# Kernel optimization log

Hardware: AMD Instinct MI355X
Metric: run time of the kernel (lower is better)

## Reference

```python
import jax, jax.numpy as jnp
import numpy as np

L = 880      # flattened RootMLP param count: (1*8+8) + (8*96+96)
HID = 8      # MLP hidden width
OUT = 96     # 2*data_size
DS = 48      # data_size
T = 64       # sequence length
BATCH = 4


def setup_inputs() -> dict:
    key = jax.random.key(0)
    k1, k2, k3, k4, k5 = jax.random.split(key, 5)
    xs = jax.random.normal(k1, (BATCH, T, DS), jnp.float32)
    ts = jax.random.uniform(k2, (BATCH, T), dtype=jnp.float32)
    theta0 = 0.1 * jax.random.normal(k3, (L,), jnp.float32)
    # near-identity A so matrix powers up to A^(T-1) stay bounded
    A = 0.99 * jnp.eye(L, dtype=jnp.float32) + (0.01 / np.sqrt(L)) * jax.random.normal(k4, (L, L), jnp.float32)
    B = 0.01 * jax.random.normal(k5, (L, DS), jnp.float32)
    return {"xs": xs, "ts": ts, "theta0": theta0, "A": A, "B": B, "aux": 0}


def _forward(xs, ts, theta0, A, B):
    Bt, T_, _ = xs.shape
    I = jnp.eye(L, dtype=A.dtype)

    # A_pows[t] = A^t for t = 0..T-1, via a cumulative matmul scan
    def step(P, _):
        return P @ A, P
    _, pows = jax.lax.scan(step, I, None, length=T_)  # (T, L, L)

    # K_conv = [B, A^0(A-I)B, ..., A^(T-3)(A-I)B]  -> (T-1, L, DS)
    M = (A - I) @ B
    K_tail = jnp.einsum('tij,jd->tid', pows[:T_ - 2], M)
    K_conv = jnp.concatenate([B[None], K_tail], axis=0)

    # FFT circular convolution of input signal with K_conv over time
    u = xs[:, 1:, :]                      # (B, T-1, DS)
    u_f = jnp.fft.fft(u, axis=1)
    K_f = jnp.fft.fft(K_conv, axis=0)     # (T-1, L, DS)
    thetas = jnp.fft.ifft(jnp.einsum('tld,btd->btl', K_f, u_f), axis=1).real

    # initial-condition convolution with K_conv0 = A^tau, tau = 0..T-2
    K0 = pows[:T_ - 1]                    # (T-1, L, L)
    sig = jnp.zeros((Bt, T_ - 1, L), xs.dtype)
    sig = sig.at[:, 0, :].set(theta0)
    sig = sig.at[:, 1, :].set(-(xs[:, 0, :] @ B.T))
    sig_f = jnp.fft.fft(sig, axis=1)
    K0_f = jnp.fft.fft(K0, axis=0)
    phi0 = jnp.fft.ifft(jnp.einsum('tlm,btm->btl', K0_f, sig_f), axis=1).real

    thetas = thetas + phi0
    thetas = jnp.concatenate([jnp.broadcast_to(theta0, (Bt, 1, L)), thetas], axis=1)  # (B, T, L)

    # apply RootMLP (1 -> HID -> OUT) with params unflattened from thetas
    W0 = thetas[..., :HID]                                    # (B,T,HID): W0 is (HID,1)
    b0 = thetas[..., HID:2 * HID]
    W1 = thetas[..., 2 * HID:2 * HID + OUT * HID].reshape(Bt, T_, OUT, HID)
    b1 = thetas[..., 2 * HID + OUT * HID:]
    h = jax.nn.relu(W0 * ts[..., None] + b0)                  # (B,T,HID)
    out = jnp.einsum('btoh,bth->bto', W1, h) + b1             # (B,T,OUT)
    # reconstruction head: tanh means, softplus stds
    return jnp.concatenate([jnp.tanh(out[..., :DS]), jax.nn.softplus(out[..., DS:])], axis=-1)


def reference(xs, ts, theta0, A, B, aux):
    return _forward(xs, ts, theta0, A, B)
```

## Files before the change

### kernel.cpp

```cpp
#include <hip/hip_runtime.h>
#include <math.h>

typedef unsigned int uint;
typedef unsigned short ushort;
typedef short s16x8 __attribute__((ext_vector_type(8)));
typedef float f32x4 __attribute__((ext_vector_type(4)));
typedef uint u32x4 __attribute__((ext_vector_type(4)));

#define L     880
#define LP    896
#define NC    64
#define WSZ   (NC * LP)
#define DS    48
#define OUTD  96
#define KCV   3072
#define NZ    6

#define OFF_E    0
#define OFF_KDT  0
#define OFF_WF   4415488
#define OFF_WB   (OFF_WF + 32 * WSZ)
#define OFF_U    (OFF_WB + 32 * WSZ / 2)
#define OFF_PART (OFF_U + 256 * KCV / 2)
#define OFF_PHI  (OFF_PART + NZ * 256 * LP)

#define LROW 72
#define LBUF (64 * LROW)
#define LGRP (2 * LBUF)

__device__ inline ushort f2b(float f) {
  uint u = __builtin_bit_cast(uint, f);
  u += 0x7fffu + ((u >> 16) & 1u);
  return (ushort)(u >> 16);
}
__device__ inline float b2f(ushort b) {
  uint u = ((uint)b) << 16;
  return __builtin_bit_cast(float, u);
}

__device__ __forceinline__ void mma_core(const ushort* __restrict__ aptr,
                                         const ushort* __restrict__ bptr,
                                         int KH, int tid, ushort* ldsA, ushort* ldsB,
                                         f32x4 acc[2][2]) {
  const int grp = tid >> 8;
  const int t2  = tid & 255;
  const int gL  = grp * LGRP;
  const int r = t2 >> 2, kq = (t2 & 3) * 16;
  const int wv = t2 >> 6, lane = tid & 63;
  const int wm = (wv >> 1) * 32, wn = (wv & 1) * 32;
  const int lr = lane & 15, lg = lane >> 4;
  acc[0][0] = f32x4{0.f, 0.f, 0.f, 0.f};
  acc[0][1] = f32x4{0.f, 0.f, 0.f, 0.f};
  acc[1][0] = f32x4{0.f, 0.f, 0.f, 0.f};
  acc[1][1] = f32x4{0.f, 0.f, 0.f, 0.f};
  u32x4 ra0 = *(const u32x4*)aptr;
  u32x4 ra1 = *(const u32x4*)(aptr + 8);
  u32x4 rb0 = *(const u32x4*)bptr;
  u32x4 rb1 = *(const u32x4*)(bptr + 8);
  __syncthreads();
  *(u32x4*)&ldsA[gL + r * LROW + kq]     = ra0;
  *(u32x4*)&ldsA[gL + r * LROW + kq + 8] = ra1;
  *(u32x4*)&ldsB[gL + r * LROW + kq]     = rb0;
  *(u32x4*)&ldsB[gL + r * LROW + kq + 8] = rb1;
  if (KH > 1) {
    ra0 = *(const u32x4*)(aptr + 64);  ra1 = *(const u32x4*)(aptr + 72);
    rb0 = *(const u32x4*)(bptr + 64);  rb1 = *(const u32x4*)(bptr + 72);
  }
  __syncthreads();
  for (int it = 0; it < KH; ++it) {
    const int cur = gL + (it & 1) * LBUF;
    const int nxt = gL + ((it & 1) ^ 1) * LBUF;
    s16x8 fa0[2], fa1[2], fb0[2], fb1[2];
#pragma unroll
    for (int k2 = 0; k2 < 2; ++k2) {
      fa0[k2] = *(const s16x8*)&ldsA[cur + (wm + lr) * LROW + k2 * 32 + lg * 8];
      fa1[k2] = *(const s16x8*)&ldsA[cur + (wm + 16 + lr) * LROW + k2 * 32 + lg * 8];
      fb0[k2] = *(const s16x8*)&ldsB[cur + (wn + lr) * LROW + k2 * 32 + lg * 8];
      fb1[k2] = *(const s16x8*)&ldsB[cur + (wn + 16 + lr) * LROW + k2 * 32 + lg * 8];
    }
    if (it + 1 < KH) {
      *(u32x4*)&ldsA[nxt + r * LROW + kq]     = ra0;
      *(u32x4*)&ldsA[nxt + r * LROW + kq + 8] = ra1;
      *(u32x4*)&ldsB[nxt + r * LROW + kq]     = rb0;
      *(u32x4*)&ldsB[nxt + r * LROW + kq + 8] = rb1;
      if (it + 2 < KH) {
        ra0 = *(const u32x4*)(aptr + (it + 2) * 64);
        ra1 = *(const u32x4*)(aptr + (it + 2) * 64 + 8);
        rb0 = *(const u32x4*)(bptr + (it + 2) * 64);
        rb1 = *(const u32x4*)(bptr + (it + 2) * 64 + 8);
      }
    }
#pragma unroll
    for (int k2 = 0; k2 < 2; ++k2) {
      acc[0][0] = __builtin_amdgcn_mfma_f32_16x16x32_bf16(fa0[k2], fb0[k2], acc[0][0], 0, 0, 0);
      acc[0][1] = __builtin_amdgcn_mfma_f32_16x16x32_bf16(fa0[k2], fb1[k2], acc[0][1], 0, 0, 0);
      acc[1][0] = __builtin_amdgcn_mfma_f32_16x16x32_bf16(fa1[k2], fb0[k2], acc[1][0], 0, 0, 0);
      acc[1][1] = __builtin_amdgcn_mfma_f32_16x16x32_bf16(fa1[k2], fb1[k2], acc[1][1], 0, 0, 0);
    }
    __syncthreads();
  }
  float* red = (float*)ldsA;
  if (grp == 1) {
#pragma unroll
    for (int m = 0; m < 2; ++m)
#pragma unroll
      for (int n = 0; n < 2; ++n)
#pragma unroll
        for (int rr = 0; rr < 4; ++rr)
          red[((m * 2 + n) * 4 + rr) * 256 + t2] = acc[m][n][rr];
  }
  __syncthreads();
  if (grp == 0) {
#pragma unroll
    for (int m = 0; m < 2; ++m)
#pragma unroll
      for (int n = 0; n < 2; ++n)
#pragma unroll
        for (int rr = 0; rr < 4; ++rr)
          acc[m][n][rr] += red[((m * 2 + n) * 4 + rr) * 256 + t2];
  }
}

__device__ __forceinline__ void mma_core_f32A(const float* __restrict__ ap1,
                                              const float* __restrict__ ap0,
                                              const ushort* __restrict__ bptr,
                                              int KH, int tid, ushort* ldsA, ushort* ldsB,
                                              f32x4 acc[2][2]) {
  const int grp = tid >> 8;
  const int t2  = tid & 255;
  const int gL  = grp * LGRP;
  const int r = t2 >> 2, kq = (t2 & 3) * 16;
  const int wv = t2 >> 6, lane = tid & 63;
  const int wm = (wv >> 1) * 32, wn = (wv & 1) * 32;
  const int lr = lane & 15, lg = lane >> 4;
  acc[0][0] = f32x4{0.f, 0.f, 0.f, 0.f};
  acc[0][1] = f32x4{0.f, 0.f, 0.f, 0.f};
  acc[1][0] = f32x4{0.f, 0.f, 0.f, 0.f};
  acc[1][1] = f32x4{0.f, 0.f, 0.f, 0.f};
  float4 ca[4], pa[4];
  auto issueA = [&](int it) {
#pragma unroll
    for (int i = 0; i < 4; ++i) {
      ca[i] = *(const float4*)(ap1 + it * 64 + i * 4);
      pa[i] = *(const float4*)(ap0 + it * 64 + i * 4);
    }
  };
  auto packA = [&](int buf) {
    union { ushort s[16]; u32x4 v[2]; } pk;
#pragma unroll
    for (int i = 0; i < 4; ++i) {
      pk.s[i * 4 + 0] = f2b(ca[i].x - pa[i].x);
      pk.s[i * 4 + 1] = f2b(ca[i].y - pa[i].y);
      pk.s[i * 4 + 2] = f2b(ca[i].z - pa[i].z);
      pk.s[i * 4 + 3] = f2b(ca[i].w - pa[i].w);
    }
    *(u32x4*)&ldsA[buf + r * LROW + kq]     = pk.v[0];
    *(u32x4*)&ldsA[buf + r * LROW + kq + 8] = pk.v[1];
  };
  u32x4 rb0 = *(const u32x4*)bptr;
  u32x4 rb1 = *(const u32x4*)(bptr + 8);
  issueA(0);
  __syncthreads();
  packA(gL);
  *(u32x4*)&ldsB[gL + r * LROW + kq]     = rb0;
  *(u32x4*)&ldsB[gL + r * LROW + kq + 8] = rb1;
  if (KH > 1) {
    rb0 = *(const u32x4*)(bptr + 64);
    rb1 = *(const u32x4*)(bptr + 72);
    issueA(1);
  }
  __syncthreads();
  for (int it = 0; it < KH; ++it) {
    const int cur = gL + (it & 1) * LBUF;
    const int nxt = gL + ((it & 1) ^ 1) * LBUF;
    s16x8 fa0[2], fa1[2], fb0[2], fb1[2];
#pragma unroll
    for (int k2 = 0; k2 < 2; ++k2) {
      fa0[k2] = *(const s16x8*)&ldsA[cur + (wm + lr) * LROW + k2 * 32 + lg * 8];
      fa1[k2] = *(const s16x8*)&ldsA[cur + (wm + 16 + lr) * LROW + k2 * 32 + lg * 8];
      fb0[k2] = *(const s16x8*)&ldsB[cur + (wn + lr) * LROW + k2 * 32 + lg * 8];
      fb1[k2] = *(const s16x8*)&ldsB[cur + (wn + 16 + lr) * LROW + k2 * 32 + lg * 8];
    }
    if (it + 1 < KH) {
      packA(nxt);
      *(u32x4*)&ldsB[nxt + r * LROW + kq]     = rb0;
      *(u32x4*)&ldsB[nxt + r * LROW + kq + 8] = rb1;
      if (it + 2 < KH) {
        rb0 = *(const u32x4*)(bptr + (it + 2) * 64);
        rb1 = *(const u32x4*)(bptr + (it + 2) * 64 + 8);
        issueA(it + 2);
      }
    }
#pragma unroll
    for (int k2 = 0; k2 < 2; ++k2) {
      acc[0][0] = __builtin_amdgcn_mfma_f32_16x16x32_bf16(fa0[k2], fb0[k2], acc[0][0], 0, 0, 0);
      acc[0][1] = __builtin_amdgcn_mfma_f32_16x16x32_bf16(fa0[k2], fb1[k2], acc[0][1], 0, 0, 0);
      acc[1][0] = __builtin_amdgcn_mfma_f32_16x16x32_bf16(fa1[k2], fb0[k2], acc[1][0], 0, 0, 0);
      acc[1][1] = __builtin_amdgcn_mfma_f32_16x16x32_bf16(fa1[k2], fb1[k2], acc[1][1], 0, 0, 0);
    }
    __syncthreads();
  }
  float* red = (float*)ldsA;
  if (grp == 1) {
#pragma unroll
    for (int m = 0; m < 2; ++m)
#pragma unroll
      for (int n = 0; n < 2; ++n)
#pragma unroll
        for (int rr = 0; rr < 4; ++rr)
          red[((m * 2 + n) * 4 + rr) * 256 + t2] = acc[m][n][rr];
  }
  __syncthreads();
  if (grp == 0) {
#pragma unroll
    for (int m = 0; m < 2; ++m)
#pragma unroll
      for (int n = 0; n < 2; ++n)
#pragma unroll
        for (int rr = 0; rr < 4; ++rr)
          acc[m][n][rr] += red[((m * 2 + n) * 4 + rr) * 256 + t2];
  }
}

__device__ __forceinline__ void kd_body(const float* __restrict__ WF, ushort* __restrict__ KDT,
                                        int j, int l0, int tid, float (*D)[65]) {
  __syncthreads();
  if (j < 63) {
    const float* Wj = WF + (size_t)j * WSZ;
    for (int e = tid; e < 48 * 64; e += 512) {
      int d = e >> 6, ll = e & 63;
      float v = Wj[d * LP + l0 + ll];
      if (j > 0) v -= Wj[-(int)WSZ + d * LP + l0 + ll];
      D[d][ll] = v;
    }
  } else {
    for (int e = tid; e < 48 * 64; e += 512) { int d = e >> 6, ll = e & 63; D[d][ll] = 0.f; }
  }
  __syncthreads();
  for (int e = tid; e < 48 * 64; e += 512) {
    int ll = e / 48, d = e - ll * 48;
    KDT[(size_t)(l0 + ll) * KCV + j * 48 + d] = f2b(D[d][ll]);
  }
}

__global__ __launch_bounds__(256) void k_prep(const float* __restrict__ A,
                                              const float* __restrict__ B,
                                              const float* __restrict__ th0,
                                              const float* __restrict__ xs,
                                              ushort* __restrict__ EN,
                                              ushort* __restrict__ ET,
                                              float* __restrict__ WF,
                                              ushort* __restrict__ WB,
                                              ushort* __restrict__ U) {
  const int blk = blockIdx.x;
  const int tid = threadIdx.x;
  if (blk < 196) {
    __shared__ float T[64][65];
    const int bi = (blk / 14) * 64, bj = (blk % 14) * 64;
    const int r = tid >> 2, c0 = (tid & 3) * 16;
    const int gi = bi + r;
#pragma unroll
    for (int q = 0; q < 4; ++q) {
      int c = c0 + q * 4, gj = bj + c;
      float4 v = {0.f, 0.f, 0.f, 0.f};
      if (gi < L && gj + 3 < L) {
        v = *(const float4*)(A + (size_t)gi * L + gj);
      } else if (gi < L) {
        if (gj + 0 < L) v.x = A[(size_t)gi * L + gj];
        if (gj + 1 < L) v.y = A[(size_t)gi * L + gj + 1];
        if (gj + 2 < L) v.z = A[(size_t)gi * L + gj + 2];
        if (gj + 3 < L) v.w = A[(size_t)gi * L + gj + 3];
      }
      if (gi == gj)     v.x -= 0.99f;
      if (gi == gj + 1) v.y -= 0.99f;
      if (gi == gj + 2) v.z -= 0.99f;
      if (gi == gj + 3) v.w -= 0.99f;
      T[r][c] = v.x; T[r][c + 1] = v.y; T[r][c + 2] = v.z; T[r][c + 3] = v.w;
    }
    __syncthreads();
    {
      union { ushort s[16]; u32x4 v[2]; } pk;
#pragma unroll
      for (int i = 0; i < 16; ++i) pk.s[i] = f2b(T[r][c0 + i]);
      *(u32x4*)(EN + (size_t)(bi + r) * LP + bj + c0)     = pk.v[0];
      *(u32x4*)(EN + (size_t)(bi + r) * LP + bj + c0 + 8) = pk.v[1];
    }
    {
      union { ushort s[16]; u32x4 v[2]; } pk;
#pragma unroll
      for (int i = 0; i < 16; ++i) pk.s[i] = f2b(T[c0 + i][r]);
      *(u32x4*)(ET + (size_t)(bj + r) * LP + bi + c0)     = pk.v[0];
      *(u32x4*)(ET + (size_t)(bj + r) * LP + bi + c0 + 8) = pk.v[1];
    }
  } else if (blk < 210) {
    int base = (blk - 196) * 4096;
    for (int e = tid; e < 4096; e += 256) {
      int idx = base + e;
      int c = idx / LP, l = idx % LP;
      float v = 0.f;
      if (l < L) {
        if (c < DS) v = B[l * DS + c];
        else if (c == DS) v = th0[l];
        else if (c < 53) {
          int b = c - 49;
          float s = 0.f;
          for (int d = 0; d < DS; ++d) s += B[l * DS + d] * xs[(b * 64) * DS + d];
          v = -s;
        }
      }
      WF[idx] = v;
      WB[idx] = f2b(v);
    }
  } else {
    int idx = ((blk - 210) * 256 + tid) * 4;
    int rr = idx / KCV, k = idx - rr * KCV;
    ushort4 v = {0, 0, 0, 0};
    if (rr < 252 && k < 3024) {
      int b = rr / 63, tau = rr - b * 63;
      int j = k / DS, d = k - j * DS;
      int s = tau - j; if (s < 0) s += 63;
      float4 x4 = *(const float4*)(xs + (size_t)(b * 64 + s + 1) * DS + d);
      v.x = f2b(x4.x); v.y = f2b(x4.y); v.z = f2b(x4.z); v.w = f2b(x4.w);
    }
    *(ushort4*)(U + idx) = v;
  }
}

__global__ __launch_bounds__(512, 4) void k_ladder(
    const ushort* __restrict__ sqA, const ushort* __restrict__ sqBT, float cs2,
    ushort* __restrict__ sqOutN, ushort* __restrict__ sqOutT, int ySq,
    int nCh, const ushort* __restrict__ chWB, const ushort* __restrict__ chE, float csc,
    const float* __restrict__ chWFsrc, float* __restrict__ chWFdst,
    ushort* __restrict__ chWBdst,
    int kdJ0, const float* __restrict__ kdWF, ushort* __restrict__ kdKDT) {
  __shared__ __align__(16) ushort ldsA[2 * LGRP];
  __shared__ __align__(16) ushort ldsB[2 * LGRP];
  const int tid = threadIdx.x;
  const int y = blockIdx.y;
  const int n0 = blockIdx.x * 64;
  const int t2 = tid & 255, grp = tid >> 8;
  const int r = t2 >> 2, kq = (t2 & 3) * 16;
  const int kg = grp * 448 + kq;
  const int wv = t2 >> 6, lane = tid & 63;
  const int wm = (wv >> 1) * 32, wn = (wv & 1) * 32;
  const int lr = lane & 15, lg = lane >> 4;

  if (y < ySq) {
    const int m0 = y * 64;
    f32x4 acc[2][2];
    mma_core(sqA + (size_t)(m0 + r) * LP + kg, sqBT + (size_t)(n0 + r) * LP + kg,
             7, tid, ldsA, ldsB, acc);
    ushort* T = ldsB;
    if (tid < 256) {
#pragma unroll
      for (int fm = 0; fm < 2; ++fm)
#pragma unroll
        for (int fn = 0; fn < 2; ++fn)
#pragma unroll
          for (int rr = 0; rr < 4; ++rr) {
            int mi = wm + fm * 16 + lg * 4 + rr;
            int ni = wn + fn * 16 + lr;
            float v = acc[fm][fn][rr] + cs2 * b2f(sqA[(size_t)(m0 + mi) * LP + n0 + ni]);
            ushort bv = f2b(v);
            sqOutN[(size_t)(m0 + mi) * LP + n0 + ni] = bv;
            T[ni * LROW + mi] = bv;
          }
    }
    __syncthreads();
    if (sqOutT && tid < 256) {
      const int nr = tid >> 2, ct0 = (tid & 3) * 16;
      u32x4 o0 = *(const u32x4*)&T[nr * LROW + ct0];
      u32x4 o1 = *(const u32x4*)&T[nr * LROW + ct0 + 8];
      *(u32x4*)(sqOutT + (size_t)(n0 + nr) * LP + m0 + ct0)     = o0;
      *(u32x4*)(sqOutT + (size_t)(n0 + nr) * LP + m0 + ct0 + 8) = o1;
    }
  } else if (y < ySq + nCh) {
    const int t = y - ySq;
    f32x4 acc[2][2];
    mma_core(chWB + (size_t)t * WSZ + (size_t)r * LP + kg,
             chE + (size_t)(n0 + r) * LP + kg, 7, tid, ldsA, ldsB, acc);
    if (tid < 256) {
      const float*  srcF = chWFsrc + (size_t)t * WSZ;
      float*        dstF = chWFdst + (size_t)t * WSZ;
      ushort*       dstB = chWBdst + (size_t)t * WSZ;
#pragma unroll
      for (int fm = 0; fm < 2; ++fm)
#pragma unroll
        for (int fn = 0; fn < 2; ++fn)
#pragma unroll
          for (int rr = 0; rr < 4; ++rr) {
            int mi = wm + fm * 16 + lg * 4 + rr;
            int ni = n0 + wn + fn * 16 + lr;
            float v = acc[fm][fn][rr] + csc * srcF[(size_t)mi * LP + ni];
            dstF[(size_t)mi * LP + ni] = v;
            dstB[(size_t)mi * LP + ni] = f2b(v);
          }
    }
  } else {
    int j = kdJ0 + (y - ySq - nCh);
    kd_body(kdWF, kdKDT, j, n0, tid, (float(*)[65])ldsA);
  }
}

__global__ __launch_bounds__(512, 4) void k_tail(
    const ushort* __restrict__ WB, const float* __restrict__ WF,
    const ushort* __restrict__ EN16, const ushort* __restrict__ EN32,
    float c16v, float c32v, float* __restrict__ PHI, ushort* __restrict__ KDT) {
  __shared__ __align__(16) ushort ldsA[2 * LGRP];
  __shared__ __align__(16) ushort ldsB[2 * LGRP];
  const int tid = threadIdx.x;
  const int y = blockIdx.y;
  const int n0 = blockIdx.x * 64;
  const int t2 = tid & 255, grp = tid >> 8;
  const int r = t2 >> 2, kq = (t2 & 3) * 16;
  const int kg = grp * 448 + kq;
  const int wv = t2 >> 6, lane = tid & 63;
  const int wm = (wv >> 1) * 32, wn = (wv & 1) * 32;
  const int lr = lane & 15, lg = lane >> 4;

  if (y < 3) {
    const int m0 = y * 64;
    int i = m0 + r; if (i > 154) i = 154;
    int t = i / 5, q = i - t * 5;
    f32x4 acc[2][2];
    mma_core(WB + (size_t)t * WSZ + (size_t)(48 + q) * LP + kg,
             EN32 + (size_t)(n0 + r) * LP + kg, 7, tid, ldsA, ldsB, acc);
    if (tid < 256) {
#pragma unroll
      for (int fm = 0; fm < 2; ++fm)
#pragma unroll
        for (int fn = 0; fn < 2; ++fn)
#pragma unroll
          for (int rr = 0; rr < 4; ++rr) {
            int mi = wm + fm * 16 + lg * 4 + rr;
            int ni = n0 + wn + fn * 16 + lr;
            int io = m0 + mi;
            int ic = io > 154 ? 154 : io;
            int tt = ic / 5, qq = ic - tt * 5;
            float v = acc[fm][fn][rr] + c32v * WF[(size_t)tt * WSZ + (size_t)(48 + qq) * LP + ni];
            PHI[(size_t)io * LP + ni] = v;
          }
    }
  } else if (y < 34) {
    const int kt = y - 3;
    const int s = (kt == 0) ? 16 : kt;
    const ushort* E = (kt == 0) ? EN16 : EN32;
    const float coef = (kt == 0) ? c16v : c32v;
    const int j = (kt == 0) ? 32 : kt + 32;
    const float* ap1 = WF + (size_t)s * WSZ + (size_t)r * LP + kg;
    f32x4 acc[2][2];
    mma_core_f32A(ap1, ap1 - WSZ, E + (size_t)(n0 + r) * LP + kg, 7, tid, ldsA, ldsB, acc);
    ushort* T = ldsB;
    if (tid < 256) {
#pragma unroll
      for (int fm = 0; fm < 2; ++fm)
#pragma unroll
        for (int fn = 0; fn < 2; ++fn)
#pragma unroll
          for (int rr = 0; rr < 4; ++rr) {
            int mi = wm + fm * 16 + lg * 4 + rr;
            if (mi < 48) {
              int ni = n0 + wn + fn * 16 + lr;
              float kds = WF[(size_t)s * WSZ + (size_t)mi * LP + ni]
                        - WF[(size_t)(s - 1) * WSZ + (size_t)mi * LP + ni];
              float v = acc[fm][fn][rr] + coef * kds;
              T[(wn + fn * 16 + lr) * LROW + mi] = f2b(v);
            }
          }
    }
    __syncthreads();
    if (tid < 384) {
      int row = tid / 6, seg = tid - row * 6;
      *(u32x4*)(KDT + (size_t)(n0 + row) * KCV + j * 48 + seg * 8)
          = *(const u32x4*)&T[row * LROW + seg * 8];
    }
  } else {
    int idx = y - 34;
    int j = (idx < 16) ? 16 + idx : 63;
    kd_body(WF, KDT, j, n0, tid, (float(*)[65])ldsA);
  }
}

__global__ __launch_bounds__(512, 4) void k_conv(const ushort* __restrict__ U,
                                                 const ushort* __restrict__ KDT,
                                                 float* __restrict__ part) {
  __shared__ __align__(16) ushort ldsA[2 * LGRP];
  __shared__ __align__(16) ushort ldsB[2 * LGRP];
  const int tid = threadIdx.x;
  const int n0 = blockIdx.x * 64, m0 = blockIdx.y * 64;
  const int t2 = tid & 255, grp = tid >> 8;
  const int r = t2 >> 2, kq = (t2 & 3) * 16;
  const int kgc = blockIdx.z * 512 + grp * 256 + kq;
  const int wv = t2 >> 6, lane = tid & 63;
  const int wm = (wv >> 1) * 32, wn = (wv & 1) * 32;
  const int lr = lane & 15, lg = lane >> 4;
  f32x4 acc[2][2];
  mma_core(U + (size_t)(m0 + r) * KCV + kgc, KDT + (size_t)(n0 + r) * KCV + kgc,
           4, tid, ldsA, ldsB, acc);
  if (tid < 256) {
    float* pp = part + (size_t)blockIdx.z * (256 * LP);
#pragma unroll
    for (int fm = 0; fm < 2; ++fm)
#pragma unroll
      for (int fn = 0; fn < 2; ++fn)
#pragma unroll
        for (int rr = 0; rr < 4; ++rr) {
          int m = m0 + wm + fm * 16 + lg * 4 + rr;
          int n = n0 + wn + fn * 16 + lr;
          pp[(size_t)m * LP + n] = acc[fm][fn][rr];
        }
  }
}

__global__ __launch_bounds__(256) void k_final(const float* __restrict__ part,
                                               const float* __restrict__ PHI,
                                               const float* __restrict__ WF,
                                               const float* __restrict__ th0,
                                               const float* __restrict__ ts,
                                               float* __restrict__ out) {
  __shared__ float th[LP];
  const int bt = blockIdx.x, b = bt >> 6, t = bt & 63;
  for (int l = threadIdx.x; l < LP; l += 256) {
    float v = 0.f;
    if (l < L) {
      if (t == 0) v = th0[l];
      else {
        int rr = b * 63 + (t - 1);
#pragma unroll
        for (int z = 0; z < NZ; ++z) v += part[(size_t)z * (256 * LP) + rr * LP + l];
        int tau = t - 1;
        v += (tau < 32) ? WF[(size_t)tau * WSZ + DS * LP + l]
                        : PHI[(size_t)((tau - 32) * 5) * LP + l];
        int tw = (tau + 62) % 63;
        v += (tw < 32) ? WF[(size_t)tw * WSZ + (49 + b) * LP + l]
                       : PHI[(size_t)((tw - 32) * 5 + 1 + b) * LP + l];
      }
    }
    th[l] = v;
  }
  __syncthreads();
  int o = threadIdx.x;
  if (o < OUTD) {
    float tv = ts[bt];
    float acc = th[784 + o];
#pragma unroll
    for (int i = 0; i < 8; ++i) {
      float h = fmaxf(th[i] * tv + th[8 + i], 0.f);
      acc += th[16 + o * 8 + i] * h;
    }
    float rs;
    if (o < DS) rs = tanhf(acc);
    else        rs = fmaxf(acc, 0.f) + log1pf(expf(-fabsf(acc)));
    out[bt * OUTD + o] = rs;
  }
}

extern "C" void kernel_launch(void* const* d_in, const int* in_sizes, int n_in,
                              void* d_out, int out_size, void* d_ws, size_t ws_size,
                              hipStream_t stream) {
  const float* xs  = (const float*)d_in[0];
  const float* ts  = (const float*)d_in[1];
  const float* th0 = (const float*)d_in[2];
  const float* A   = (const float*)d_in[3];
  const float* B   = (const float*)d_in[4];
  float* out = (float*)d_out;
  float* ws  = (float*)d_ws;

  ushort* EP   = (ushort*)(ws + OFF_E);
  const size_t PL = (size_t)LP * LP;
  ushort* EN1  = EP + 0 * PL;
  ushort* ET1  = EP + 1 * PL;
  ushort* EN2  = EP + 2 * PL;
  ushort* ET2  = EP + 3 * PL;
  ushort* EN4  = EP + 4 * PL;
  ushort* ET4  = EP + 5 * PL;
  ushort* EN8  = EP + 6 * PL;
  ushort* ET8  = EP + 7 * PL;
  ushort* EN16 = EP + 8 * PL;
  ushort* ET16 = EP + 9 * PL;
  ushort* EN32 = EP + 10 * PL;
  float*  WF   = ws + OFF_WF;
  ushort* WB   = (ushort*)(ws + OFF_WB);
  ushort* KDT  = (ushort*)(ws + OFF_KDT);
  ushort* U    = (ushort*)(ws + OFF_U);
  float*  part = ws + OFF_PART;
  float*  PHI  = ws + OFF_PHI;

  const float c1 = 0.99f;
  const float c2 = c1 * c1, c4 = c2 * c2, c8 = c4 * c4, c16 = c8 * c8, c32 = c16 * c16;

  k_prep<<<978, 256, 0, stream>>>(A, B, th0, xs, EN1, ET1, WF, WB, U);

  k_ladder<<<dim3(14, 15), 512, 0, stream>>>(EN1, ET1, 2.f * c1, EN2, ET2, 14,
                                             1, WB, EN1, c1, WF, WF + 1 * WSZ, WB + (size_t)1 * WSZ,
                                             0, nullptr, nullptr);
  k_ladder<<<dim3(14, 16), 512, 0, stream>>>(EN2, ET2, 2.f * c2, EN4, ET4, 14,
                                             2, WB, EN2, c2, WF, WF + 2 * WSZ, WB + (size_t)2 * WSZ,
                                             0, nullptr, nullptr);
  k_ladder<<<dim3(14, 18), 512, 0, stream>>>(EN4, ET4, 2.f * c4, EN8, ET8, 14,
                                             4, WB, EN4, c4, WF, WF + 4 * WSZ, WB + (size_t)4 * WSZ,
                                             0, nullptr, nullptr);
  k_ladder<<<dim3(14, 22), 512, 0, stream>>>(EN8, ET8, 2.f * c8, EN16, ET16, 14,
                                             8, WB, EN8, c8, WF, WF + 8 * WSZ, WB + (size_t)8 * WSZ,
                                             0, nullptr, nullptr);
  k_ladder<<<dim3(14, 46), 512, 0, stream>>>(EN16, ET16, 2.f * c16, EN32, nullptr, 14,
                                             16, WB, EN16, c16, WF, WF + 16 * WSZ, WB + (size_t)16 * WSZ,
                                             0, WF, KDT);
  k_tail<<<dim3(14, 51), 512, 0, stream>>>(WB, WF, EN16, EN32, c16, c32, PHI, KDT);

  k_conv<<<dim3(14, 4, NZ), 512, 0, stream>>>(U, KDT, part);
  k_final<<<256, 256, 0, stream>>>(part, PHI, WF, th0, ts, out);
}
```

Before: 96.67 us.

## Rebalance ladder tail stages and fuse early conv splits into tail kernel

Replaces the last ladder launch with a new mid kernel that computes EN32, the upper half of the power chain, KDT columns 0-15 and the chained KDT columns 16-31. The tail kernel now also handles KDT column 63 and the first three k-splits of the convolution GEMM, which only need KDT columns already written by earlier launches. The standalone conv kernel keeps only the remaining three k-splits. This is meant to spread the work more evenly across launches and fill otherwise idle blocks. The cost is more branch variety per kernel and a tighter dependency ordering that must be correct.

```diff
diff --git a/kernel.cpp b/kernel.cpp
--- a/kernel.cpp
+++ b/kernel.cpp
@@ -222,6 +222,45 @@
   }
 }
 
+__device__ __forceinline__ void kdchain_task(const float* __restrict__ WF,
+                                             const ushort* __restrict__ E, float coef,
+                                             int s, int j, int n0, int tid, int kg,
+                                             ushort* ldsA, ushort* ldsB,
+                                             ushort* __restrict__ KDT) {
+  const int t2 = tid & 255;
+  const int r = t2 >> 2;
+  const int wv = t2 >> 6, lane = tid & 63;
+  const int wm = (wv >> 1) * 32, wn = (wv & 1) * 32;
+  const int lr = lane & 15, lg = lane >> 4;
+  const float* ap1 = WF + (size_t)s * WSZ + (size_t)r * LP + kg;
+  f32x4 acc[2][2];
+  mma_core_f32A(ap1, ap1 - WSZ, E + (size_t)(n0 + r) * LP + kg, 7, tid, ldsA, ldsB, acc);
+  ushort* T = ldsB;
+  if (tid < 256) {
+#pragma unroll
+    for (int fm = 0; fm < 2; ++fm)
+#pragma unroll
+      for (int fn = 0; fn < 2; ++fn)
+#pragma unroll
+        for (int rr = 0; rr < 4; ++rr) {
+          int mi = wm + fm * 16 + lg * 4 + rr;
+          if (mi < 48) {
+            int ni = n0 + wn + fn * 16 + lr;
+            float kds = WF[(size_t)s * WSZ + (size_t)mi * LP + ni]
+                      - WF[(size_t)(s - 1) * WSZ + (size_t)mi * LP + ni];
+            float v = acc[fm][fn][rr] + coef * kds;
+            T[(wn + fn * 16 + lr) * LROW + mi] = f2b(v);
+          }
+        }
+  }
+  __syncthreads();
+  if (tid < 384) {
+    int row = tid / 6, seg = tid - row * 6;
+    *(u32x4*)(KDT + (size_t)(n0 + row) * KCV + j * 48 + seg * 8)
+        = *(const u32x4*)&T[row * LROW + seg * 8];
+  }
+}
+
 __device__ __forceinline__ void kd_body(const float* __restrict__ WF, ushort* __restrict__ KDT,
                                         int j, int l0, int tid, float (*D)[65]) {
   __syncthreads();
@@ -331,8 +370,7 @@
     ushort* __restrict__ sqOutN, ushort* __restrict__ sqOutT, int ySq,
     int nCh, const ushort* __restrict__ chWB, const ushort* __restrict__ chE, float csc,
     const float* __restrict__ chWFsrc, float* __restrict__ chWFdst,
-    ushort* __restrict__ chWBdst,
-    int kdJ0, const float* __restrict__ kdWF, ushort* __restrict__ kdKDT) {
+    ushort* __restrict__ chWBdst) {
   __shared__ __align__(16) ushort ldsA[2 * LGRP];
   __shared__ __align__(16) ushort ldsB[2 * LGRP];
   const int tid = threadIdx.x;
@@ -374,7 +412,7 @@
       *(u32x4*)(sqOutT + (size_t)(n0 + nr) * LP + m0 + ct0)     = o0;
       *(u32x4*)(sqOutT + (size_t)(n0 + nr) * LP + m0 + ct0 + 8) = o1;
     }
-  } else if (y < ySq + nCh) {
+  } else {
     const int t = y - ySq;
     f32x4 acc[2][2];
     mma_core(chWB + (size_t)t * WSZ + (size_t)r * LP + kg,
@@ -396,16 +434,15 @@
             dstB[(size_t)mi * LP + ni] = f2b(v);
           }
     }
-  } else {
-    int j = kdJ0 + (y - ySq - nCh);
-    kd_body(kdWF, kdKDT, j, n0, tid, (float(*)[65])ldsA);
-  }
-}
-
-__global__ __launch_bounds__(512, 4) void k_tail(
-    const ushort* __restrict__ WB, const float* __restrict__ WF,
-    const ushort* __restrict__ EN16, const ushort* __restrict__ EN32,
-    float c16v, float c32v, float* __restrict__ PHI, ushort* __restrict__ KDT) {
+  }
+}
+
+__global__ __launch_bounds__(512, 4) void k_mid(
+    const ushort* __restrict__ EN8, const ushort* __restrict__ EN16,
+    const ushort* __restrict__ ET16, ushort* __restrict__ EN32,
+    float c8v, float c16v,
+    ushort* __restrict__ WB, float* __restrict__ WF,
+    ushort* __restrict__ KDT) {
   __shared__ __align__(16) ushort ldsA[2 * LGRP];
   __shared__ __align__(16) ushort ldsB[2 * LGRP];
   const int tid = threadIdx.x;
@@ -418,6 +455,73 @@
   const int wm = (wv >> 1) * 32, wn = (wv & 1) * 32;
   const int lr = lane & 15, lg = lane >> 4;
 
+  if (y < 14) {
+    const int m0 = y * 64;
+    f32x4 acc[2][2];
+    mma_core(EN16 + (size_t)(m0 + r) * LP + kg, ET16 + (size_t)(n0 + r) * LP + kg,
+             7, tid, ldsA, ldsB, acc);
+    if (tid < 256) {
+#pragma unroll
+      for (int fm = 0; fm < 2; ++fm)
+#pragma unroll
+        for (int fn = 0; fn < 2; ++fn)
+#pragma unroll
+          for (int rr = 0; rr < 4; ++rr) {
+            int mi = wm + fm * 16 + lg * 4 + rr;
+            int ni = wn + fn * 16 + lr;
+            float v = acc[fm][fn][rr] + 2.f * c16v * b2f(EN16[(size_t)(m0 + mi) * LP + n0 + ni]);
+            EN32[(size_t)(m0 + mi) * LP + n0 + ni] = f2b(v);
+          }
+    }
+  } else if (y < 30) {
+    const int t = y - 14;
+    f32x4 acc[2][2];
+    mma_core(WB + (size_t)t * WSZ + (size_t)r * LP + kg,
+             EN16 + (size_t)(n0 + r) * LP + kg, 7, tid, ldsA, ldsB, acc);
+    if (tid < 256) {
+      const float*  srcF = WF + (size_t)t * WSZ;
+      float*        dstF = WF + (size_t)(t + 16) * WSZ;
+      ushort*       dstB = WB + (size_t)(t + 16) * WSZ;
+#pragma unroll
+      for (int fm = 0; fm < 2; ++fm)
+#pragma unroll
+        for (int fn = 0; fn < 2; ++fn)
+#pragma unroll
+          for (int rr = 0; rr < 4; ++rr) {
+            int mi = wm + fm * 16 + lg * 4 + rr;
+            int ni = n0 + wn + fn * 16 + lr;
+            float v = acc[fm][fn][rr] + c16v * srcF[(size_t)mi * LP + ni];
+            dstF[(size_t)mi * LP + ni] = v;
+            dstB[(size_t)mi * LP + ni] = f2b(v);
+          }
+    }
+  } else if (y < 46) {
+    kd_body(WF, KDT, y - 30, n0, tid, (float(*)[65])ldsA);
+  } else if (y == 46) {
+    kdchain_task(WF, EN8, c8v, 8, 16, n0, tid, kg, ldsA, ldsB, KDT);
+  } else {
+    int j = 17 + (y - 47);
+    kdchain_task(WF, EN16, c16v, j - 16, j, n0, tid, kg, ldsA, ldsB, KDT);
+  }
+}
+
+__global__ __launch_bounds__(512, 4) void k_tail(
+    const ushort* __restrict__ WB, const float* __restrict__ WF,
+    const ushort* __restrict__ EN16, const ushort* __restrict__ EN32,
+    float c16v, float c32v, float* __restrict__ PHI, ushort* __restrict__ KDT,
+    const ushort* __restrict__ U, float* __restrict__ part) {
+  __shared__ __align__(16) ushort ldsA[2 * LGRP];
+  __shared__ __align__(16) ushort ldsB[2 * LGRP];
+  const int tid = threadIdx.x;
+  const int y = blockIdx.y;
+  const int n0 = blockIdx.x * 64;
+  const int t2 = tid & 255, grp = tid >> 8;
+  const int r = t2 >> 2, kq = (t2 & 3) * 16;
+  const int kg = grp * 448 + kq;
+  const int wv = t2 >> 6, lane = tid & 63;
+  const int wm = (wv >> 1) * 32, wn = (wv & 1) * 32;
+  const int lr = lane & 15, lg = lane >> 4;
+
   if (y < 3) {
     const int m0 = y * 64;
     int i = m0 + r; if (i > 154) i = 154;
@@ -443,41 +547,30 @@
     }
   } else if (y < 34) {
     const int kt = y - 3;
-    const int s = (kt == 0) ? 16 : kt;
-    const ushort* E = (kt == 0) ? EN16 : EN32;
-    const float coef = (kt == 0) ? c16v : c32v;
-    const int j = (kt == 0) ? 32 : kt + 32;
-    const float* ap1 = WF + (size_t)s * WSZ + (size_t)r * LP + kg;
+    if (kt == 0) kdchain_task(WF, EN16, c16v, 16, 32, n0, tid, kg, ldsA, ldsB, KDT);
+    else         kdchain_task(WF, EN32, c32v, kt, kt + 32, n0, tid, kg, ldsA, ldsB, KDT);
+  } else if (y == 34) {
+    kd_body(WF, KDT, 63, n0, tid, (float(*)[65])ldsA);
+  } else {
+    const int c = y - 35;
+    const int z = c >> 2, m0 = (c & 3) * 64;
+    const int kgc = z * 512 + grp * 256 + kq;
     f32x4 acc[2][2];
-    mma_core_f32A(ap1, ap1 - WSZ, E + (size_t)(n0 + r) * LP + kg, 7, tid, ldsA, ldsB, acc);
-    ushort* T = ldsB;
+    mma_core(U + (size_t)(m0 + r) * KCV + kgc, KDT + (size_t)(n0 + r) * KCV + kgc,
+             4, tid, ldsA, ldsB, acc);
     if (tid < 256) {
+      float* pp = part + (size_t)z * (256 * LP);
 #pragma unroll
       for (int fm = 0; fm < 2; ++fm)
 #pragma unroll
         for (int fn = 0; fn < 2; ++fn)
 #pragma unroll
           for (int rr = 0; rr < 4; ++rr) {
-            int mi = wm + fm * 16 + lg * 4 + rr;
-            if (mi < 48) {
-              int ni = n0 + wn + fn * 16 + lr;
-              float kds = WF[(size_t)s * WSZ + (size_t)mi * LP + ni]
-                        - WF[(size_t)(s - 1) * WSZ + (size_t)mi * LP + ni];
-              float v = acc[fm][fn][rr] + coef * kds;
-              T[(wn + fn * 16 + lr) * LROW + mi] = f2b(v);
-            }
+            int m = m0 + wm + fm * 16 + lg * 4 + rr;
+            int n = n0 + wn + fn * 16 + lr;
+            pp[(size_t)m * LP + n] = acc[fm][fn][rr];
           }
     }
-    __syncthreads();
-    if (tid < 384) {
-      int row = tid / 6, seg = tid - row * 6;
-      *(u32x4*)(KDT + (size_t)(n0 + row) * KCV + j * 48 + seg * 8)
-          = *(const u32x4*)&T[row * LROW + seg * 8];
-    }
-  } else {
-    int idx = y - 34;
-    int j = (idx < 16) ? 16 + idx : 63;
-    kd_body(WF, KDT, j, n0, tid, (float(*)[65])ldsA);
   }
 }
 
@@ -488,9 +581,10 @@
   __shared__ __align__(16) ushort ldsB[2 * LGRP];
   const int tid = threadIdx.x;
   const int n0 = blockIdx.x * 64, m0 = blockIdx.y * 64;
+  const int z = 3 + blockIdx.z;
   const int t2 = tid & 255, grp = tid >> 8;
   const int r = t2 >> 2, kq = (t2 & 3) * 16;
-  const int kgc = blockIdx.z * 512 + grp * 256 + kq;
+  const int kgc = z * 512 + grp * 256 + kq;
   const int wv = t2 >> 6, lane = tid & 63;
   const int wm = (wv >> 1) * 32, wn = (wv & 1) * 32;
   const int lr = lane & 15, lg = lane >> 4;
@@ -498,7 +592,7 @@
   mma_core(U + (size_t)(m0 + r) * KCV + kgc, KDT + (size_t)(n0 + r) * KCV + kgc,
            4, tid, ldsA, ldsB, acc);
   if (tid < 256) {
-    float* pp = part + (size_t)blockIdx.z * (256 * LP);
+    float* pp = part + (size_t)z * (256 * LP);
 #pragma unroll
     for (int fm = 0; fm < 2; ++fm)
 #pragma unroll
@@ -592,22 +686,15 @@
   k_prep<<<978, 256, 0, stream>>>(A, B, th0, xs, EN1, ET1, WF, WB, U);
 
   k_ladder<<<dim3(14, 15), 512, 0, stream>>>(EN1, ET1, 2.f * c1, EN2, ET2, 14,
-                                             1, WB, EN1, c1, WF, WF + 1 * WSZ, WB + (size_t)1 * WSZ,
-                                             0, nullptr, nullptr);
+                                             1, WB, EN1, c1, WF, WF + 1 * WSZ, WB + (size_t)1 * WSZ);
   k_ladder<<<dim3(14, 16), 512, 0, stream>>>(EN2, ET2, 2.f * c2, EN4, ET4, 14,
-                                             2, WB, EN2, c2, WF, WF + 2 * WSZ, WB + (size_t)2 * WSZ,
-                                             0, nullptr, nullptr);
+                                             2, WB, EN2, c2, WF, WF + 2 * WSZ, WB + (size_t)2 * WSZ);
   k_ladder<<<dim3(14, 18), 512, 0, stream>>>(EN4, ET4, 2.f * c4, EN8, ET8, 14,
-                                             4, WB, EN4, c4, WF, WF + 4 * WSZ, WB + (size_t)4 * WSZ,
-                                             0, nullptr, nullptr);
+                                             4, WB, EN4, c4, WF, WF + 4 * WSZ, WB + (size_t)4 * WSZ);
   k_ladder<<<dim3(14, 22), 512, 0, stream>>>(EN8, ET8, 2.f * c8, EN16, ET16, 14,
-                                             8, WB, EN8, c8, WF, WF + 8 * WSZ, WB + (size_t)8 * WSZ,
-                                             0, nullptr, nullptr);
-  k_ladder<<<dim3(14, 46), 512, 0, stream>>>(EN16, ET16, 2.f * c16, EN32, nullptr, 14,
-                                             16, WB, EN16, c16, WF, WF + 16 * WSZ, WB + (size_t)16 * WSZ,
-                                             0, WF, KDT);
-  k_tail<<<dim3(14, 51), 512, 0, stream>>>(WB, WF, EN16, EN32, c16, c32, PHI, KDT);
-
-  k_conv<<<dim3(14, 4, NZ), 512, 0, stream>>>(U, KDT, part);
+                                             8, WB, EN8, c8, WF, WF + 8 * WSZ, WB + (size_t)8 * WSZ);
+  k_mid<<<dim3(14, 62), 512, 0, stream>>>(EN8, EN16, ET16, EN32, c8, c16, WB, WF, KDT);
+  k_tail<<<dim3(14, 47), 512, 0, stream>>>(WB, WF, EN16, EN32, c16, c32, PHI, KDT, U, part);
+  k_conv<<<dim3(14, 4, 3), 512, 0, stream>>>(U, KDT, part);
   k_final<<<256, 256, 0, stream>>>(part, PHI, WF, th0, ts, out);
 }
```

Result: slower. 108.7 us (+12.5%).
